# Kernel optimization log

Measured on AMD Instinct MI355X. Metric: run time of the kernel, lower is better.

Reference implementation:

```python
import jax, jax.numpy as jnp
import numpy as np

N = 8192
F_IN = 256
F_OUT = 256
EDGE_P = 0.002  # avg degree ~16 before self-loops


def setup_inputs() -> dict:
    key = jax.random.key(0)
    k_a, k_x, k_w, k_b = jax.random.split(key, 4)
    # symmetric 0/1 dense adjacency, no self loops (added in reference as I + A)
    u = jax.random.uniform(k_a, (N, N))
    A = (u < EDGE_P).astype(jnp.float32)
    A = jnp.maximum(A, A.T)
    A = A * (1.0 - jnp.eye(N, dtype=jnp.float32))
    inputs = jax.random.normal(k_x, (N, F_IN), dtype=jnp.float32)
    # matches torch init: rand/100 - 0.005 in [-0.005, 0.005)
    weight = jax.random.uniform(k_w, (F_IN, F_OUT), dtype=jnp.float32) / 100.0 - 0.005
    bias = jax.random.uniform(k_b, (F_OUT,), dtype=jnp.float32) / 100.0 - 0.005
    return {"A": A, "inputs": inputs, "weight": weight, "bias": bias}


def reference(A, inputs, weight, bias):
    # A_ = I + A
    A_ = A + jnp.eye(A.shape[0], dtype=A.dtype)
    # D^{-1/2}: the original builds diag matrices and does dense GEMMs;
    # row/col scaling is the same math, expressed efficiently.
    d = jnp.sum(A_, axis=1) ** (-0.5)  # [N]
    norm_A = d[:, None] * A_ * d[None, :]  # D^{-1/2} (I+A) D^{-1/2}
    out = norm_A @ inputs @ weight + bias  # [N, F_OUT]
    return out  # activation is None
```

## Files before the change

kernel.cpp:

```cpp
#include <hip/hip_runtime.h>
#include <hip/hip_bf16.h>
#include <cstdint>


#define NN 8192
#define FF 256
#define ELLK 128
#define BM 64
#define BN 64
#define NGEMM ((NN / BM) * (FF / BN))

typedef short bf16x8 __attribute__((ext_vector_type(8)));
typedef float f32x4  __attribute__((ext_vector_type(4)));

__device__ __forceinline__ float bf2f(unsigned short u) {
    union { unsigned int i; float f; } c; c.i = ((unsigned int)u) << 16; return c.f;
}
__device__ __forceinline__ unsigned short f2bf(float f) {
    union { float f; unsigned int i; } c; c.f = f;
    unsigned int r = c.i + 0x7FFF + ((c.i >> 16) & 1);
    return (unsigned short)(r >> 16);
}

__global__ __launch_bounds__(256) void fused_stage1(const float* __restrict__ A,
                                                    const float* __restrict__ X,
                                                    const float* __restrict__ W,
                                                    unsigned short* __restrict__ Yb,
                                                    int* __restrict__ cnt,
                                                    unsigned short* __restrict__ ell) {
    if (blockIdx.x < NGEMM) {
        __shared__ unsigned short Xs[64][68];
        __shared__ unsigned short Wt[64][68];
        const int bid = blockIdx.x;
        const int m0 = (bid / (FF / BN)) * BM;
        const int n0 = (bid % (FF / BN)) * BN;
        const int t  = threadIdx.x;
        const int w  = t >> 6;
        const int l  = t & 63;
        const int lm = l & 15;
        const int lk = (l >> 4) << 2;
        f32x4 acc[4] = {};
        for (int kp = 0; kp < 4; ++kp) {
            const int kbase = kp * 64;
            __syncthreads();
            {
                int row = t >> 2;
                #pragma unroll
                for (int q = 0; q < 4; ++q) {
                    int kq = (t & 3) * 4 + q * 16;
                    float4 v = *reinterpret_cast<const float4*>(X + (size_t)(m0 + row) * FF + kbase + kq);
                    ushort4 b = { f2bf(v.x), f2bf(v.y), f2bf(v.z), f2bf(v.w) };
                    *reinterpret_cast<ushort4*>(&Xs[row][kq]) = b;
                }
            }
            {
                int n4 = (t & 15) * 4;
                int kk = t >> 4;
                #pragma unroll
                for (int q = 0; q < 4; ++q) {
                    int k = kk + q * 16;
                    float4 v = *reinterpret_cast<const float4*>(W + (size_t)(kbase + k) * FF + n0 + n4);
                    Wt[n4 + 0][k] = f2bf(v.x);
                    Wt[n4 + 1][k] = f2bf(v.y);
                    Wt[n4 + 2][k] = f2bf(v.z);
                    Wt[n4 + 3][k] = f2bf(v.w);
                }
            }
            __syncthreads();
            #pragma unroll
            for (int ks = 0; ks < 2; ++ks) {
                const int k0 = ks * 32;
                union { bf16x8 v; uint2 u[2]; } af;
                af.u[0] = *reinterpret_cast<const uint2*>(&Xs[w * 16 + lm][k0 + lk]);
                af.u[1] = *reinterpret_cast<const uint2*>(&Xs[w * 16 + lm][k0 + 16 + lk]);
                #pragma unroll
                for (int f = 0; f < 4; ++f) {
                    union { bf16x8 v; uint2 u[2]; } bf;
                    bf.u[0] = *reinterpret_cast<const uint2*>(&Wt[f * 16 + lm][k0 + lk]);
                    bf.u[1] = *reinterpret_cast<const uint2*>(&Wt[f * 16 + lm][k0 + 16 + lk]);
                    acc[f] = __builtin_amdgcn_mfma_f32_16x16x32_bf16(af.v, bf.v, acc[f], 0, 0, 0);
                }
            }
        }
        #pragma unroll
        for (int f = 0; f < 4; ++f) {
            #pragma unroll
            for (int r = 0; r < 4; ++r) {
                int row = m0 + w * 16 + lk + r;
                int col = n0 + f * 16 + lm;
                Yb[(size_t)row * FF + col] = f2bf(acc[f][r]);
            }
        }
    } else {
        __shared__ unsigned short loc[ELLK];
        __shared__ int lcnt, base;
        const int r = blockIdx.x - NGEMM;
        if (threadIdx.x == 0) lcnt = 0;
        __syncthreads();
        const uint4* Arow = reinterpret_cast<const uint4*>(A + (size_t)r * NN);
        const int c0 = (r + 1) >> 2;
        for (int c = c0 + threadIdx.x; c < NN / 4; c += 256) {
            uint4 v = Arow[c];
            if (v.x | v.y | v.z | v.w) {
                int b = c * 4;
                if (v.x && b + 0 > r) { int p = atomicAdd(&lcnt, 1); if (p < ELLK) loc[p] = (unsigned short)(b + 0); }
                if (v.y && b + 1 > r) { int p = atomicAdd(&lcnt, 1); if (p < ELLK) loc[p] = (unsigned short)(b + 1); }
                if (v.z && b + 2 > r) { int p = atomicAdd(&lcnt, 1); if (p < ELLK) loc[p] = (unsigned short)(b + 2); }
                if (v.w && b + 3 > r) { int p = atomicAdd(&lcnt, 1); if (p < ELLK) loc[p] = (unsigned short)(b + 3); }
            }
        }
        __syncthreads();
        const int n = lcnt < ELLK ? lcnt : ELLK;
        if (threadIdx.x == 0) base = atomicAdd(&cnt[r], n);
        __syncthreads();
        for (int t = threadIdx.x; t < n; t += 256) {
            int p = base + t;
            if (p < ELLK) ell[(size_t)r * ELLK + p] = loc[t];
        }
        for (int t = threadIdx.x; t < n; t += 256) {
            int j = loc[t];
            int q = atomicAdd(&cnt[j], 1);
            if (q < ELLK) ell[(size_t)j * ELLK + q] = (unsigned short)r;
        }
    }
}

__global__ __launch_bounds__(256) void spmm_kernel(const unsigned short* __restrict__ Yb,
                                                   const int* __restrict__ cnt,
                                                   const unsigned short* __restrict__ ell,
                                                   const float* __restrict__ bias,
                                                   float* __restrict__ out) {
    const int wave = threadIdx.x >> 6;
    const int lane = threadIdx.x & 63;
    const int row = blockIdx.x * 4 + wave;
    __shared__ unsigned short sidx[4][ELLK];
    __shared__ float sdj[4][ELLK];
    int c = cnt[row];
    c = c < ELLK ? c : ELLK;
    for (int t = lane; t < c; t += 64) {
        int j = ell[(size_t)row * ELLK + t];
        sidx[wave][t] = (unsigned short)j;
        sdj[wave][t]  = rsqrtf((float)(cnt[j] + 1));
    }
    __syncthreads();
    const float di = rsqrtf((float)(c + 1));
    ushort4 ys = *reinterpret_cast<const ushort4*>(Yb + (size_t)row * FF + lane * 4);
    float a0 = di * bf2f(ys.x), a1 = di * bf2f(ys.y);
    float a2 = di * bf2f(ys.z), a3 = di * bf2f(ys.w);
    for (int t = 0; t < c; ++t) {
        int j = sidx[wave][t];
        float dj = sdj[wave][t];
        ushort4 v = *reinterpret_cast<const ushort4*>(Yb + (size_t)j * FF + lane * 4);
        a0 = fmaf(dj, bf2f(v.x), a0);
        a1 = fmaf(dj, bf2f(v.y), a1);
        a2 = fmaf(dj, bf2f(v.z), a2);
        a3 = fmaf(dj, bf2f(v.w), a3);
    }
    float4 b4 = *reinterpret_cast<const float4*>(bias + lane * 4);
    float4 o;
    o.x = fmaf(di, a0, b4.x);
    o.y = fmaf(di, a1, b4.y);
    o.z = fmaf(di, a2, b4.z);
    o.w = fmaf(di, a3, b4.w);
    *reinterpret_cast<float4*>(out + (size_t)row * FF + lane * 4) = o;
}

extern "C" void kernel_launch(void* const* d_in, const int* in_sizes, int n_in,
                              void* d_out, int out_size, void* d_ws, size_t ws_size,
                              hipStream_t stream) {
    const float* A    = (const float*)d_in[0];
    const float* X    = (const float*)d_in[1];
    const float* W    = (const float*)d_in[2];
    const float* bias = (const float*)d_in[3];
    float* out = (float*)d_out;

    char* ws = (char*)d_ws;
    unsigned short* Yb  = (unsigned short*)(ws);
    int*            cnt = (int*)(ws + (size_t)NN * FF * 2);
    unsigned short* ell = (unsigned short*)(ws + (size_t)NN * FF * 2 + NN * 4);

    hipMemsetAsync(cnt, 0, NN * sizeof(int), stream);

    fused_stage1<<<NGEMM + NN, 256, 0, stream>>>(A, X, W, Yb, cnt, ell);
    spmm_kernel<<<NN / 4, 256, 0, stream>>>(Yb, cnt, ell, bias, out);
}
```

Measured before the change: 54.49 us.

## Bucket transposed edges and distribute them with shared-memory atomics

Rows no longer scatter mirrored lower-triangle edges straight into the ELL table with global atomics on per-row counters. Each row now writes its own upper-triangle neighbours directly, then appends packed (j,r) pairs into 256 bucket buffers. A new distribute kernel reads each bucket and places the entries using shared-memory atomics. The goal is to cut contention on scattered global atomics, at the cost of an extra kernel launch and an intermediate buffer with a fixed capacity per bucket.

```diff
diff --git a/kernel.cpp b/kernel.cpp
--- a/kernel.cpp
+++ b/kernel.cpp
@@ -9,6 +9,9 @@
 #define BM 64
 #define BN 64
 #define NGEMM ((NN / BM) * (FF / BN))
+#define NBUCK 256
+#define BROWS (NN / NBUCK)
+#define BCAP  2048
 
 typedef short bf16x8 __attribute__((ext_vector_type(8)));
 typedef float f32x4  __attribute__((ext_vector_type(4)));
@@ -26,8 +29,10 @@
                                                     const float* __restrict__ X,
                                                     const float* __restrict__ W,
                                                     unsigned short* __restrict__ Yb,
-                                                    int* __restrict__ cnt,
-                                                    unsigned short* __restrict__ ell) {
+                                                    int* __restrict__ fcnt,
+                                                    unsigned short* __restrict__ ell,
+                                                    int* __restrict__ bcnt,
+                                                    unsigned int* __restrict__ bbuf) {
     if (blockIdx.x < NGEMM) {
         __shared__ unsigned short Xs[64][68];
         __shared__ unsigned short Wt[64][68];
@@ -93,7 +98,7 @@
         }
     } else {
         __shared__ unsigned short loc[ELLK];
-        __shared__ int lcnt, base;
+        __shared__ int lcnt;
         const int r = blockIdx.x - NGEMM;
         if (threadIdx.x == 0) lcnt = 0;
         __syncthreads();
@@ -111,18 +116,39 @@
         }
         __syncthreads();
         const int n = lcnt < ELLK ? lcnt : ELLK;
-        if (threadIdx.x == 0) base = atomicAdd(&cnt[r], n);
-        __syncthreads();
-        for (int t = threadIdx.x; t < n; t += 256) {
-            int p = base + t;
-            if (p < ELLK) ell[(size_t)r * ELLK + p] = loc[t];
-        }
+        if (threadIdx.x == 0) fcnt[r] = n;
+        for (int t = threadIdx.x; t < n; t += 256)
+            ell[(size_t)r * ELLK + t] = loc[t];
         for (int t = threadIdx.x; t < n; t += 256) {
             int j = loc[t];
-            int q = atomicAdd(&cnt[j], 1);
-            if (q < ELLK) ell[(size_t)j * ELLK + q] = (unsigned short)r;
-        }
-    }
+            int b = j >> 5;
+            int s = atomicAdd(&bcnt[b], 1);
+            if (s < BCAP) bbuf[(size_t)b * BCAP + s] = ((unsigned int)j << 16) | (unsigned int)r;
+        }
+    }
+}
+
+__global__ __launch_bounds__(256) void distribute_kernel(const int* __restrict__ fcnt,
+                                                         const int* __restrict__ bcnt,
+                                                         const unsigned int* __restrict__ bbuf,
+                                                         int* __restrict__ cnt,
+                                                         unsigned short* __restrict__ ell) {
+    const int b = blockIdx.x;
+    __shared__ int lcnt[BROWS];
+    if (threadIdx.x < BROWS)
+        lcnt[threadIdx.x] = fcnt[b * BROWS + threadIdx.x];
+    __syncthreads();
+    const int m = bcnt[b] < BCAP ? bcnt[b] : BCAP;
+    for (int t = threadIdx.x; t < m; t += 256) {
+        unsigned int e = bbuf[(size_t)b * BCAP + t];
+        int j = e >> 16;
+        int r = e & 0xFFFF;
+        int p = atomicAdd(&lcnt[j & (BROWS - 1)], 1);
+        if (p < ELLK) ell[(size_t)j * ELLK + p] = (unsigned short)r;
+    }
+    __syncthreads();
+    if (threadIdx.x < BROWS)
+        cnt[b * BROWS + threadIdx.x] = lcnt[threadIdx.x];
 }
 
 __global__ __launch_bounds__(256) void spmm_kernel(const unsigned short* __restrict__ Yb,
@@ -175,12 +201,16 @@
     float* out = (float*)d_out;
 
     char* ws = (char*)d_ws;
-    unsigned short* Yb  = (unsigned short*)(ws);
-    int*            cnt = (int*)(ws + (size_t)NN * FF * 2);
-    unsigned short* ell = (unsigned short*)(ws + (size_t)NN * FF * 2 + NN * 4);
-
-    hipMemsetAsync(cnt, 0, NN * sizeof(int), stream);
-
-    fused_stage1<<<NGEMM + NN, 256, 0, stream>>>(A, X, W, Yb, cnt, ell);
+    unsigned short* Yb   = (unsigned short*)(ws);
+    int*            fcnt = (int*)(ws + (size_t)NN * FF * 2);
+    int*            cnt  = (int*)(ws + (size_t)NN * FF * 2 + NN * 4);
+    int*            bcnt = (int*)(ws + (size_t)NN * FF * 2 + NN * 8);
+    unsigned int*   bbuf = (unsigned int*)(ws + (size_t)NN * FF * 2 + NN * 8 + 1024);
+    unsigned short* ell  = (unsigned short*)(ws + (size_t)NN * FF * 2 + NN * 8 + 1024 + (size_t)NBUCK * BCAP * 4);
+
+    hipMemsetAsync(bcnt, 0, NBUCK * sizeof(int), stream);
+
+    fused_stage1<<<NGEMM + NN, 256, 0, stream>>>(A, X, W, Yb, fcnt, ell, bcnt, (unsigned int*)bbuf);
+    distribute_kernel<<<NBUCK, 256, 0, stream>>>(fcnt, bcnt, bbuf, cnt, ell);
     spmm_kernel<<<NN / 4, 256, 0, stream>>>(Yb, cnt, ell, bias, out);
 }
```

Result: slower. 177.4 us (+225.5%).
